# Kernel tuning notes

Hardware: AMD Instinct MI355X
Metric: run time of the kernel (lower is better)

Reference implementation:

```python
import jax, jax.numpy as jnp
import numpy as np

B, T, E, H = 4, 4096, 1024, 64

def setup_inputs() -> dict:
    key = jax.random.key(0)
    k1, k2, k3, k4 = jax.random.split(key, 4)
    x = jax.random.normal(k1, (B, T, E), dtype=jnp.float32)
    # nn.Linear(E, H, bias=False): weight [H, E]; store as [E, H] for x @ W
    scale = 1.0 / np.sqrt(E)
    Wk = jax.random.normal(k2, (E, H), dtype=jnp.float32) * scale
    Wq = jax.random.normal(k3, (E, H), dtype=jnp.float32) * scale
    Wv = jax.random.normal(k4, (E, H), dtype=jnp.float32) * scale
    return {"x": x, "Wk": Wk, "Wq": Wq, "Wv": Wv}

def reference(x, Wk, Wq, Wv):
    Bc, Tc, Ec = x.shape
    k = x @ Wk            # [B, T, H]
    q = x @ Wq            # [B, T, H]
    v = x @ Wv            # [B, T, H]
    # NOTE: original scales by 1/sqrt(embedding_size), not head_size
    scores = jnp.einsum('bqh,bkh->bqk', q, k) / jnp.sqrt(jnp.float32(Ec))
    causal = jnp.tril(jnp.ones((Tc, Tc), dtype=bool))
    scores = jnp.where(causal, scores, -jnp.inf)
    weights = jax.nn.softmax(scores, axis=-1)
    return jnp.einsum('bqk,bkh->bqh', weights, v)
```

## Files before the change

### kernel.cpp

```cpp
#include <hip/hip_runtime.h>

#define B_ 4
#define T_ 4096
#define E_ 1024
#define H_ 64

typedef __attribute__((ext_vector_type(8))) short short8;
typedef __attribute__((ext_vector_type(4))) float f32x4;

static __device__ __forceinline__ unsigned short f2bf(float f) {
    unsigned int u = __builtin_bit_cast(unsigned int, f);
    u += 0x7fffu + ((u >> 16) & 1u);
    return (unsigned short)(u >> 16);
}
static __device__ __forceinline__ float bf2f(unsigned short h) {
    unsigned int u = ((unsigned int)h) << 16;
    return __builtin_bit_cast(float, u);
}
#if __has_builtin(__builtin_amdgcn_exp2f)
#define EXP2(x) __builtin_amdgcn_exp2f(x)
#else
#define EXP2(x) exp2f(x)
#endif

#define GLOBAL_AS __attribute__((address_space(1)))
#define LDS_AS    __attribute__((address_space(3)))

__global__ __launch_bounds__(256) void wt_transpose_kernel(
    const float* __restrict__ Wq, const float* __restrict__ Wk,
    const float* __restrict__ Wv, unsigned short* __restrict__ Wt)
{
    __shared__ float tile[64][65];
    const int mat = blockIdx.x >> 4;
    const int kt  = blockIdx.x & 15;
    const float* W = (mat == 0) ? Wq : ((mat == 1) ? Wk : Wv);
    const int tid = threadIdx.x;
    #pragma unroll
    for (int p = 0; p < 16; ++p) {
        int idx = p * 256 + tid;
        tile[idx >> 6][idx & 63] = W[(kt * 64 + (idx >> 6)) * 64 + (idx & 63)];
    }
    __syncthreads();
    #pragma unroll
    for (int p = 0; p < 16; ++p) {
        int idx = p * 256 + tid;
        int h = idx >> 6, kl = idx & 63;
        Wt[(mat * 64 + h) * E_ + kt * 64 + kl] = f2bf(tile[kl][h]);
    }
}

__global__ __launch_bounds__(768, 1) void proj_kernel(
    const float* __restrict__ x, const unsigned short* __restrict__ Wt,
    unsigned short* __restrict__ Qb, unsigned short* __restrict__ Kb,
    unsigned short* __restrict__ Vt)
{
    __shared__ float          x_lds[2][4096];
    __shared__ unsigned short wt_lds[2][12288];
    const int tid  = threadIdx.x;
    const int wid  = tid >> 6, lane = tid & 63;
    const int g    = lane >> 4, c = lane & 15;
    const int mat  = wid >> 2;
    const int rg   = wid & 3;
    const int r0   = blockIdx.x * 64;
    const float QSCALE = 0.03125f * 1.44269504088896f;

    auto stage = [&](int buf, int kk) {
        {
            int row = tid >> 4, ch = tid & 15;
            int csw = ch ^ (row & 15);
            const float* src = x + (size_t)(r0 + row) * E_ + kk + csw * 4;
            __builtin_amdgcn_global_load_lds(
                (const GLOBAL_AS unsigned int*)src,
                (LDS_AS unsigned int*)&x_lds[buf][(tid & ~63) * 4], 16, 0, 0);
            if (tid < 256) {
                int idx2 = 768 + tid;
                int row2 = idx2 >> 4, ch2 = idx2 & 15;
                int csw2 = ch2 ^ (row2 & 15);
                const float* src2 = x + (size_t)(r0 + row2) * E_ + kk + csw2 * 4;
                __builtin_amdgcn_global_load_lds(
                    (const GLOBAL_AS unsigned int*)src2,
                    (LDS_AS unsigned int*)&x_lds[buf][(idx2 & ~63) * 4], 16, 0, 0);
            }
        }
        #pragma unroll
        for (int p = 0; p < 2; ++p) {
            int idx = p * 768 + tid;
            int row = idx >> 3, ch = idx & 7;
            int csw = ch ^ (row & 7);
            const unsigned short* src = Wt + (size_t)row * E_ + kk + csw * 8;
            __builtin_amdgcn_global_load_lds(
                (const GLOBAL_AS unsigned int*)src,
                (LDS_AS unsigned int*)&wt_lds[buf][(idx & ~63) * 8], 16, 0, 0);
        }
    };

    f32x4 acc[4];
    #pragma unroll
    for (int n = 0; n < 4; ++n) acc[n] = 0.0f;

    stage(0, 0);
    __syncthreads();

    for (int t = 0; t < 16; ++t) {
        const int buf = t & 1;
        if (t < 15) stage(buf ^ 1, (t + 1) * 64);

        const int xrowbase = (rg * 16 + c) * 64;
        const int wrowbase = (mat * 64 + c) * 64;
        #pragma unroll
        for (int kc = 0; kc < 2; ++kc) {
            f32x4 xa = *(const f32x4*)&x_lds[buf][xrowbase + ((8 * kc + 2 * g)     ^ c) * 4];
            f32x4 xb = *(const f32x4*)&x_lds[buf][xrowbase + ((8 * kc + 2 * g + 1) ^ c) * 4];
            short8 a;
            #pragma unroll
            for (int j = 0; j < 4; ++j) {
                a[j]     = (short)f2bf(xa[j]);
                a[j + 4] = (short)f2bf(xb[j]);
            }
            #pragma unroll
            for (int n = 0; n < 4; ++n) {
                short8 b = *(const short8*)
                    &wt_lds[buf][wrowbase + n * 1024 + (((4 * kc + g) ^ (c & 7)) * 8)];
                acc[n] = __builtin_amdgcn_mfma_f32_16x16x32_bf16(a, b, acc[n], 0, 0, 0);
            }
        }
        __syncthreads();
    }

    const int bb = r0 >> 12;
    #pragma unroll
    for (int n = 0; n < 4; ++n)
        #pragma unroll
        for (int r = 0; r < 4; ++r) {
            int row = r0 + rg * 16 + 4 * g + r;
            int col = n * 16 + c;
            float v = acc[n][r];
            if (mat == 0)
                Qb[(size_t)row * H_ + col] = f2bf(v * QSCALE);
            else if (mat == 1)
                Kb[(size_t)row * H_ + col] = f2bf(v);
            else
                Vt[((size_t)bb * H_ + col) * T_ + (row & (T_ - 1))] = f2bf(v);
        }
}

__global__ __launch_bounds__(256, 3) void attn_split_kernel(
    const unsigned short* __restrict__ Qb, const unsigned short* __restrict__ Kb,
    const unsigned short* __restrict__ Vt, unsigned short* __restrict__ Po,
    float* __restrict__ Pl)
{
    __shared__ unsigned short K_lds[2][64][64];
    __shared__ unsigned short V_lds[2][64][64];
    __shared__ unsigned short p_lds[4][16][72];
    const int tid   = threadIdx.x;
    const int wid   = tid >> 6, lane = tid & 63;
    const int g     = lane >> 4, c = lane & 15;

    const int s     = blockIdx.x * 4 + wid;
    const int batch = s >> 11;
    const int rem   = s & 2047;
    const int ch    = rem >> 8;
    const int qt    = rem & 255;
    const int nkv   = (qt >> 2) + 1;
    if (ch * 8 >= nkv) return;
    const int nt    = min(8, nkv - ch * 8);
    const int qbase = qt * 16;
    const int lastt = nkv - 1 - ch * 8;

    const int Mm = nkv - 1, aa = Mm >> 3, rr8 = Mm & 7;
    const int npart = (nkv + 7) >> 3;
    const int slot  = batch * 1152 + 4 * (4 * aa * (aa + 1) + rr8 * (aa + 1))
                    + (qt & 3) * npart + ch;

    const int rsub = lane >> 3;
    const int csw  = (lane & 7) ^ rsub;
    const int cs0 = (g ^ (c & 7)) * 8;
    const int cs1 = ((g + 4) ^ (c & 7)) * 8;

    short8 aq0, aq1;
    {
        const unsigned short* qp = Qb + ((size_t)(batch * T_ + qbase + c)) * H_ + 8 * g;
        aq0 = *(const short8*)&qp[0];
        aq1 = *(const short8*)&qp[32];
    }

    short8 ones;
    #pragma unroll
    for (int j = 0; j < 8; ++j) ones[j] = (short)0x3F80;

    f32x4 o_acc[4];
    #pragma unroll
    for (int n = 0; n < 4; ++n) o_acc[n] = 0.0f;
    f32x4 l_acc = 0.0f;

    auto stage = [&](int buf, int gt) {
        const int key0 = gt * 64;
        #pragma unroll
        for (int j = 0; j < 2; ++j) {
            const int row = wid * 16 + j * 8;
            const unsigned short* gk = Kb
                + ((size_t)(batch * T_ + key0 + row + rsub)) * H_ + csw * 8;
            __builtin_amdgcn_global_load_lds(
                (const GLOBAL_AS unsigned int*)gk,
                (LDS_AS unsigned int*)&K_lds[buf][row][0], 16, 0, 0);
            const unsigned short* gv = Vt
                + ((size_t)(batch * H_ + row + rsub)) * T_ + key0 + csw * 8;
            __builtin_amdgcn_global_load_lds(
                (const GLOBAL_AS unsigned int*)gv,
                (LDS_AS unsigned int*)&V_lds[buf][row][0], 16, 0, 0);
        }
    };

    stage(0, ch * 8);
    __syncthreads();

    for (int t = 0; t < nt; ++t) {
        const int buf = t & 1;
        if (t + 1 < nt) stage(buf ^ 1, ch * 8 + t + 1);

        f32x4 sA[4];
        #pragma unroll
        for (int n = 0; n < 4; ++n) sA[n] = 0.0f;
        #pragma unroll
        for (int n = 0; n < 4; ++n) {
            short8 bk0 = *(const short8*)&K_lds[buf][n * 16 + c][cs0];
            short8 bk1 = *(const short8*)&K_lds[buf][n * 16 + c][cs1];
            sA[n] = __builtin_amdgcn_mfma_f32_16x16x32_bf16(aq0, bk0, sA[n], 0, 0, 0);
            sA[n] = __builtin_amdgcn_mfma_f32_16x16x32_bf16(aq1, bk1, sA[n], 0, 0, 0);
        }

        float pv[4][4];
        #pragma unroll
        for (int n = 0; n < 4; ++n)
            #pragma unroll
            for (int r = 0; r < 4; ++r)
                pv[n][r] = EXP2(sA[n][r]);
        if (t == lastt) {
            const int d = (ch * 8 + t) * 64 + c - qbase - 4 * g;
            #pragma unroll
            for (int n = 0; n < 4; ++n)
                #pragma unroll
                for (int r = 0; r < 4; ++r)
                    if (d + 16 * n > r) pv[n][r] = 0.0f;
        }

        #pragma unroll
        for (int n = 0; n < 4; ++n)
            #pragma unroll
            for (int r = 0; r < 4; ++r)
                p_lds[wid][4 * g + r][n * 16 + c] = f2bf(pv[n][r]);
        short8 pa0 = *(const short8*)&p_lds[wid][c][8 * g];
        short8 pa1 = *(const short8*)&p_lds[wid][c][32 + 8 * g];

        l_acc = __builtin_amdgcn_mfma_f32_16x16x32_bf16(pa0, ones, l_acc, 0, 0, 0);
        l_acc = __builtin_amdgcn_mfma_f32_16x16x32_bf16(pa1, ones, l_acc, 0, 0, 0);

        #pragma unroll
        for (int n = 0; n < 4; ++n) {
            short8 bv0 = *(const short8*)&V_lds[buf][n * 16 + c][cs0];
            short8 bv1 = *(const short8*)&V_lds[buf][n * 16 + c][cs1];
            o_acc[n] = __builtin_amdgcn_mfma_f32_16x16x32_bf16(pa0, bv0, o_acc[n], 0, 0, 0);
            o_acc[n] = __builtin_amdgcn_mfma_f32_16x16x32_bf16(pa1, bv1, o_acc[n], 0, 0, 0);
        }

        __syncthreads();
    }

    unsigned short* po = Po + (size_t)slot * 1024;
    #pragma unroll
    for (int n = 0; n < 4; ++n)
        #pragma unroll
        for (int r = 0; r < 4; ++r)
            po[(4 * g + r) * 64 + n * 16 + c] = f2bf(o_acc[n][r]);
    if (c == 0) {
        #pragma unroll
        for (int r = 0; r < 4; ++r)
            Pl[slot * 16 + 4 * g + r] = l_acc[r];
    }
}

__global__ __launch_bounds__(256) void attn_merge_kernel(
    const unsigned short* __restrict__ Po, const float* __restrict__ Pl,
    float* __restrict__ out)
{
    const int tid  = threadIdx.x;
    const int wid  = tid >> 6, lane = tid & 63;
    const int gi   = blockIdx.x * 4 + wid;
    const int batch = gi >> 8, qt = gi & 255;
    const int nkv  = (qt >> 2) + 1;
    const int npart = (nkv + 7) >> 3;
    const int Mm = nkv - 1, aa = Mm >> 3, rr8 = Mm & 7;
    const int slot0 = batch * 1152 + 4 * (4 * aa * (aa + 1) + rr8 * (aa + 1))
                    + (qt & 3) * npart;

    const int row = lane & 15, seg = lane >> 4;

    float lacc = 0.0f, o[16];
    #pragma unroll
    for (int k = 0; k < 16; ++k) o[k] = 0.0f;

    for (int i = 0; i < npart; ++i) {
        lacc += Pl[(slot0 + i) * 16 + row];
        const unsigned short* pp = Po + (size_t)(slot0 + i) * 1024 + row * 64 + seg * 16;
        short8 v0 = *(const short8*)&pp[0];
        short8 v1 = *(const short8*)&pp[8];
        #pragma unroll
        for (int k = 0; k < 8; ++k) {
            o[k]     += bf2f((unsigned short)v0[k]);
            o[8 + k] += bf2f((unsigned short)v1[k]);
        }
    }

    const float inv = 1.0f / lacc;
    float* op = out + ((size_t)(batch * T_ + qt * 16 + row)) * H_ + seg * 16;
    #pragma unroll
    for (int k = 0; k < 16; ++k) op[k] = o[k] * inv;
}

extern "C" void kernel_launch(void* const* d_in, const int* in_sizes, int n_in,
                              void* d_out, int out_size, void* d_ws, size_t ws_size,
                              hipStream_t stream)
{
    const float* x  = (const float*)d_in[0];
    const float* Wk = (const float*)d_in[1];
    const float* Wq = (const float*)d_in[2];
    const float* Wv = (const float*)d_in[3];
    float* out = (float*)d_out;

    unsigned short* Wt = (unsigned short*)d_ws;
    unsigned short* Qb = Wt + 3 * 64 * 1024;
    unsigned short* Kb = Qb + (size_t)B_ * T_ * H_;
    unsigned short* Vt = Kb + (size_t)B_ * T_ * H_;
    unsigned short* Po = Vt + (size_t)B_ * T_ * H_;
    float* Pl = (float*)(Po + (size_t)4608 * 1024);

    hipLaunchKernelGGL(wt_transpose_kernel, dim3(48), dim3(256), 0, stream, Wq, Wk, Wv, Wt);
    hipLaunchKernelGGL(proj_kernel, dim3(256), dim3(768), 0, stream, x, Wt, Qb, Kb, Vt);
    hipLaunchKernelGGL(attn_split_kernel, dim3(2048), dim3(256), 0, stream, Qb, Kb, Vt, Po, Pl);
    hipLaunchKernelGGL(attn_merge_kernel, dim3(256), dim3(256), 0, stream, Po, Pl, out);
}
```

Measured before the change: 67.94 us.

## Load x directly into registers and pipeline weight staging with manual waitcnt

The projection kernel stops staging x through LDS and has each wave load its x rows from global memory straight into registers, double-buffered one step ahead. Weight tiles are still staged in LDS, and the loop is unrolled by two with explicit s_waitcnt vmcnt and s_barrier in place of __syncthreads. This cuts LDS traffic and barrier cost, but each x row is now fetched by the three matrix waves separately, which adds global/L2 reads.

```diff
diff --git a/kernel.cpp b/kernel.cpp
--- a/kernel.cpp
+++ b/kernel.cpp
@@ -54,7 +54,6 @@
     unsigned short* __restrict__ Qb, unsigned short* __restrict__ Kb,
     unsigned short* __restrict__ Vt)
 {
-    __shared__ float          x_lds[2][4096];
     __shared__ unsigned short wt_lds[2][12288];
     const int tid  = threadIdx.x;
     const int wid  = tid >> 6, lane = tid & 63;
@@ -64,24 +63,9 @@
     const int r0   = blockIdx.x * 64;
     const float QSCALE = 0.03125f * 1.44269504088896f;
 
-    auto stage = [&](int buf, int kk) {
-        {
-            int row = tid >> 4, ch = tid & 15;
-            int csw = ch ^ (row & 15);
-            const float* src = x + (size_t)(r0 + row) * E_ + kk + csw * 4;
-            __builtin_amdgcn_global_load_lds(
-                (const GLOBAL_AS unsigned int*)src,
-                (LDS_AS unsigned int*)&x_lds[buf][(tid & ~63) * 4], 16, 0, 0);
-            if (tid < 256) {
-                int idx2 = 768 + tid;
-                int row2 = idx2 >> 4, ch2 = idx2 & 15;
-                int csw2 = ch2 ^ (row2 & 15);
-                const float* src2 = x + (size_t)(r0 + row2) * E_ + kk + csw2 * 4;
-                __builtin_amdgcn_global_load_lds(
-                    (const GLOBAL_AS unsigned int*)src2,
-                    (LDS_AS unsigned int*)&x_lds[buf][(idx2 & ~63) * 4], 16, 0, 0);
-            }
-        }
+    const float* xrow = x + (size_t)(r0 + rg * 16 + c) * E_;
+
+    auto stageWt = [&](int buf, int kk) {
         #pragma unroll
         for (int p = 0; p < 2; ++p) {
             int idx = p * 768 + tid;
@@ -93,29 +77,27 @@
                 (LDS_AS unsigned int*)&wt_lds[buf][(idx & ~63) * 8], 16, 0, 0);
         }
     };
+    auto loadx = [&](f32x4* dst, int t) {
+        const float* xr = xrow + t * 64;
+        dst[0] = *(const f32x4*)&xr[8 * g];
+        dst[1] = *(const f32x4*)&xr[8 * g + 4];
+        dst[2] = *(const f32x4*)&xr[32 + 8 * g];
+        dst[3] = *(const f32x4*)&xr[32 + 8 * g + 4];
+    };
 
     f32x4 acc[4];
     #pragma unroll
     for (int n = 0; n < 4; ++n) acc[n] = 0.0f;
 
-    stage(0, 0);
-    __syncthreads();
-
-    for (int t = 0; t < 16; ++t) {
-        const int buf = t & 1;
-        if (t < 15) stage(buf ^ 1, (t + 1) * 64);
-
-        const int xrowbase = (rg * 16 + c) * 64;
-        const int wrowbase = (mat * 64 + c) * 64;
+    const int wrowbase = (mat * 64 + c) * 64;
+    auto computeStep = [&](int buf, const f32x4* xs) {
         #pragma unroll
         for (int kc = 0; kc < 2; ++kc) {
-            f32x4 xa = *(const f32x4*)&x_lds[buf][xrowbase + ((8 * kc + 2 * g)     ^ c) * 4];
-            f32x4 xb = *(const f32x4*)&x_lds[buf][xrowbase + ((8 * kc + 2 * g + 1) ^ c) * 4];
             short8 a;
             #pragma unroll
             for (int j = 0; j < 4; ++j) {
-                a[j]     = (short)f2bf(xa[j]);
-                a[j + 4] = (short)f2bf(xb[j]);
+                a[j]     = (short)f2bf(xs[kc * 2][j]);
+                a[j + 4] = (short)f2bf(xs[kc * 2 + 1][j]);
             }
             #pragma unroll
             for (int n = 0; n < 4; ++n) {
@@ -124,7 +106,31 @@
                 acc[n] = __builtin_amdgcn_mfma_f32_16x16x32_bf16(a, b, acc[n], 0, 0, 0);
             }
         }
-        __syncthreads();
+    };
+
+    f32x4 xA[4], xB[4];
+    stageWt(0, 0);
+    asm volatile("" ::: "memory");
+    loadx(xA, 0);
+    asm volatile("s_waitcnt vmcnt(0)\n\ts_barrier" ::: "memory");
+
+    #pragma unroll
+    for (int tt = 0; tt < 16; tt += 2) {
+        stageWt(1, (tt + 1) * 64);
+        asm volatile("" ::: "memory");
+        loadx(xB, tt + 1);
+        computeStep(0, xA);
+        asm volatile("s_waitcnt vmcnt(4)\n\ts_barrier" ::: "memory");
+
+        if (tt + 2 < 16) {
+            stageWt(0, (tt + 2) * 64);
+            asm volatile("" ::: "memory");
+            loadx(xA, tt + 2);
+            computeStep(1, xB);
+            asm volatile("s_waitcnt vmcnt(4)\n\ts_barrier" ::: "memory");
+        } else {
+            computeStep(1, xB);
+        }
     }
 
     const int bb = r0 >> 12;
```

New measurement: 74.11 us. 9.1% more time.

## Split projection GEMM along K into two halves with a merge kernel

Applied to the files above, without the earlier changes.

The projection kernel now splits the 1024-wide reduction into two halves, doubling the grid from 256 to 512 blocks so more CUs get work. Each half writes bf16 partial sums to workspace, and a new merge kernel adds them, applies the Q scale and writes Q, K and transposed V. This costs an extra kernel launch, an extra round trip of partials through memory, and an extra bf16 rounding of the partial sums. The launch-bounds hint also changes.

```diff
diff --git a/kernel.cpp b/kernel.cpp
--- a/kernel.cpp
+++ b/kernel.cpp
@@ -49,10 +49,9 @@
     }
 }
 
-__global__ __launch_bounds__(768, 1) void proj_kernel(
+__global__ __launch_bounds__(768, 6) void proj_kernel(
     const float* __restrict__ x, const unsigned short* __restrict__ Wt,
-    unsigned short* __restrict__ Qb, unsigned short* __restrict__ Kb,
-    unsigned short* __restrict__ Vt)
+    unsigned short* __restrict__ Pp)
 {
     __shared__ float          x_lds[2][4096];
     __shared__ unsigned short wt_lds[2][12288];
@@ -61,8 +60,10 @@
     const int g    = lane >> 4, c = lane & 15;
     const int mat  = wid >> 2;
     const int rg   = wid & 3;
-    const int r0   = blockIdx.x * 64;
-    const float QSCALE = 0.03125f * 1.44269504088896f;
+    const int mtile = blockIdx.x >> 1;
+    const int kh    = blockIdx.x & 1;
+    const int r0   = mtile * 64;
+    const int k0   = kh * 512;
 
     auto stage = [&](int buf, int kk) {
         {
@@ -98,15 +99,9 @@
     #pragma unroll
     for (int n = 0; n < 4; ++n) acc[n] = 0.0f;
 
-    stage(0, 0);
-    __syncthreads();
-
-    for (int t = 0; t < 16; ++t) {
-        const int buf = t & 1;
-        if (t < 15) stage(buf ^ 1, (t + 1) * 64);
-
-        const int xrowbase = (rg * 16 + c) * 64;
-        const int wrowbase = (mat * 64 + c) * 64;
+    const int xrowbase = (rg * 16 + c) * 64;
+    const int wrowbase = (mat * 64 + c) * 64;
+    auto computeStep = [&](int buf) {
         #pragma unroll
         for (int kc = 0; kc < 2; ++kc) {
             f32x4 xa = *(const f32x4*)&x_lds[buf][xrowbase + ((8 * kc + 2 * g)     ^ c) * 4];
@@ -124,24 +119,60 @@
                 acc[n] = __builtin_amdgcn_mfma_f32_16x16x32_bf16(a, b, acc[n], 0, 0, 0);
             }
         }
+    };
+
+    stage(0, k0);
+    __syncthreads();
+    for (int t = 0; t < 8; ++t) {
+        const int buf = t & 1;
+        if (t + 1 < 8) stage(buf ^ 1, k0 + (t + 1) * 64);
+        computeStep(buf);
         __syncthreads();
     }
 
-    const int bb = r0 >> 12;
+    unsigned short* pp = Pp + ((size_t)kh * 16384 + r0) * 192;
     #pragma unroll
     for (int n = 0; n < 4; ++n)
         #pragma unroll
-        for (int r = 0; r < 4; ++r) {
-            int row = r0 + rg * 16 + 4 * g + r;
-            int col = n * 16 + c;
-            float v = acc[n][r];
-            if (mat == 0)
-                Qb[(size_t)row * H_ + col] = f2bf(v * QSCALE);
-            else if (mat == 1)
-                Kb[(size_t)row * H_ + col] = f2bf(v);
-            else
-                Vt[((size_t)bb * H_ + col) * T_ + (row & (T_ - 1))] = f2bf(v);
-        }
+        for (int r = 0; r < 4; ++r)
+            pp[(rg * 16 + 4 * g + r) * 192 + mat * 64 + n * 16 + c] = f2bf(acc[n][r]);
+}
+
+__global__ __launch_bounds__(256) void qkv_merge_kernel(
+    const unsigned short* __restrict__ Pp,
+    unsigned short* __restrict__ Qb, unsigned short* __restrict__ Kb,
+    unsigned short* __restrict__ Vt)
+{
+    const float QSCALE = 0.03125f * 1.44269504088896f;
+    const int idx   = blockIdx.x * 256 + threadIdx.x;
+    const int row   = idx / 24;
+    const int chunk = idx - row * 24;
+
+    short8 a = *(const short8*)&Pp[(size_t)row * 192 + chunk * 8];
+    short8 b = *(const short8*)&Pp[((size_t)16384 + row) * 192 + chunk * 8];
+    float s[8];
+    #pragma unroll
+    for (int j = 0; j < 8; ++j)
+        s[j] = bf2f((unsigned short)a[j]) + bf2f((unsigned short)b[j]);
+
+    if (chunk < 8) {
+        short8 v;
+        #pragma unroll
+        for (int j = 0; j < 8; ++j) v[j] = (short)f2bf(s[j] * QSCALE);
+        *(short8*)&Qb[(size_t)row * H_ + chunk * 8] = v;
+    } else if (chunk < 16) {
+        short8 v;
+        #pragma unroll
+        for (int j = 0; j < 8; ++j) v[j] = (short)f2bf(s[j]);
+        *(short8*)&Kb[(size_t)row * H_ + (chunk - 8) * 8] = v;
+    } else {
+        const int col0 = (chunk - 16) * 8;
+        const int bb   = row >> 12;
+        const int rloc = row & (T_ - 1);
+        #pragma unroll
+        for (int j = 0; j < 8; ++j)
+            Vt[((size_t)(bb * H_ + col0 + j)) * T_ + rloc] = f2bf(s[j]);
+    }
 }
 
 __global__ __launch_bounds__(256, 3) void attn_split_kernel(
@@ -331,11 +362,14 @@
     unsigned short* Qb = Wt + 3 * 64 * 1024;
     unsigned short* Kb = Qb + (size_t)B_ * T_ * H_;
     unsigned short* Vt = Kb + (size_t)B_ * T_ * H_;
-    unsigned short* Po = Vt + (size_t)B_ * T_ * H_;
+    unsigned short* U  = Vt + (size_t)B_ * T_ * H_;
+    unsigned short* Pp = U;
+    unsigned short* Po = U;
     float* Pl = (float*)(Po + (size_t)4608 * 1024);
 
     hipLaunchKernelGGL(wt_transpose_kernel, dim3(48), dim3(256), 0, stream, Wq, Wk, Wv, Wt);
-    hipLaunchKernelGGL(proj_kernel, dim3(256), dim3(768), 0, stream, x, Wt, Qb, Kb, Vt);
+    hipLaunchKernelGGL(proj_kernel, dim3(512), dim3(768), 0, stream, x, Wt, Pp);
+    hipLaunchKernelGGL(qkv_merge_kernel, dim3(1536), dim3(256), 0, stream, Pp, Qb, Kb, Vt);
     hipLaunchKernelGGL(attn_split_kernel, dim3(2048), dim3(256), 0, stream, Qb, Kb, Vt, Po, Pl);
     hipLaunchKernelGGL(attn_merge_kernel, dim3(256), dim3(256), 0, stream, Po, Pl, out);
 }
```

Result: faster. 64.72 us (-4.7%).

## Split projection kernel into per-matrix 256-thread blocks for more parallelism

Applied to the files above, without the earlier changes.

The fused 768-thread block that computed Q, K and V for a 64-row tile becomes three 256-thread blocks, one per weight matrix. The grid grows from 256 to 768 blocks, which fills more CUs on the chip and allows up to three blocks per CU, with smaller LDS per block. The cost is that each x tile is loaded from global memory three times instead of once, tripling x traffic for the projection.

```diff
diff --git a/kernel.cpp b/kernel.cpp
--- a/kernel.cpp
+++ b/kernel.cpp
@@ -49,45 +49,38 @@
     }
 }
 
-__global__ __launch_bounds__(768, 1) void proj_kernel(
+__global__ __launch_bounds__(256, 3) void proj_kernel(
     const float* __restrict__ x, const unsigned short* __restrict__ Wt,
     unsigned short* __restrict__ Qb, unsigned short* __restrict__ Kb,
     unsigned short* __restrict__ Vt)
 {
     __shared__ float          x_lds[2][4096];
-    __shared__ unsigned short wt_lds[2][12288];
+    __shared__ unsigned short wt_lds[2][4096];
     const int tid  = threadIdx.x;
-    const int wid  = tid >> 6, lane = tid & 63;
+    const int rg   = tid >> 6, lane = tid & 63;
     const int g    = lane >> 4, c = lane & 15;
-    const int mat  = wid >> 2;
-    const int rg   = wid & 3;
-    const int r0   = blockIdx.x * 64;
+    const int bx   = blockIdx.x;
+    const int mtile = bx / 3, mat = bx - mtile * 3;
+    const int r0   = mtile * 64;
     const float QSCALE = 0.03125f * 1.44269504088896f;
 
     auto stage = [&](int buf, int kk) {
-        {
-            int row = tid >> 4, ch = tid & 15;
+        #pragma unroll
+        for (int p = 0; p < 4; ++p) {
+            int idx = p * 256 + tid;
+            int row = idx >> 4, ch = idx & 15;
             int csw = ch ^ (row & 15);
             const float* src = x + (size_t)(r0 + row) * E_ + kk + csw * 4;
             __builtin_amdgcn_global_load_lds(
                 (const GLOBAL_AS unsigned int*)src,
-                (LDS_AS unsigned int*)&x_lds[buf][(tid & ~63) * 4], 16, 0, 0);
-            if (tid < 256) {
-                int idx2 = 768 + tid;
-                int row2 = idx2 >> 4, ch2 = idx2 & 15;
-                int csw2 = ch2 ^ (row2 & 15);
-                const float* src2 = x + (size_t)(r0 + row2) * E_ + kk + csw2 * 4;
-                __builtin_amdgcn_global_load_lds(
-                    (const GLOBAL_AS unsigned int*)src2,
-                    (LDS_AS unsigned int*)&x_lds[buf][(idx2 & ~63) * 4], 16, 0, 0);
-            }
+                (LDS_AS unsigned int*)&x_lds[buf][(idx & ~63) * 4], 16, 0, 0);
         }
         #pragma unroll
         for (int p = 0; p < 2; ++p) {
-            int idx = p * 768 + tid;
+            int idx = p * 256 + tid;
             int row = idx >> 3, ch = idx & 7;
             int csw = ch ^ (row & 7);
-            const unsigned short* src = Wt + (size_t)row * E_ + kk + csw * 8;
+            const unsigned short* src = Wt + (size_t)(mat * 64 + row) * E_ + kk + csw * 8;
             __builtin_amdgcn_global_load_lds(
                 (const GLOBAL_AS unsigned int*)src,
                 (LDS_AS unsigned int*)&wt_lds[buf][(idx & ~63) * 8], 16, 0, 0);
@@ -98,15 +91,8 @@
     #pragma unroll
     for (int n = 0; n < 4; ++n) acc[n] = 0.0f;
 
-    stage(0, 0);
-    __syncthreads();
-
-    for (int t = 0; t < 16; ++t) {
-        const int buf = t & 1;
-        if (t < 15) stage(buf ^ 1, (t + 1) * 64);
-
-        const int xrowbase = (rg * 16 + c) * 64;
-        const int wrowbase = (mat * 64 + c) * 64;
+    const int xrowbase = (rg * 16 + c) * 64;
+    auto computeStep = [&](int buf) {
         #pragma unroll
         for (int kc = 0; kc < 2; ++kc) {
             f32x4 xa = *(const f32x4*)&x_lds[buf][xrowbase + ((8 * kc + 2 * g)     ^ c) * 4];
@@ -120,10 +106,18 @@
             #pragma unroll
             for (int n = 0; n < 4; ++n) {
                 short8 b = *(const short8*)
-                    &wt_lds[buf][wrowbase + n * 1024 + (((4 * kc + g) ^ (c & 7)) * 8)];
+                    &wt_lds[buf][(n * 16 + c) * 64 + (((4 * kc + g) ^ (c & 7)) * 8)];
                 acc[n] = __builtin_amdgcn_mfma_f32_16x16x32_bf16(a, b, acc[n], 0, 0, 0);
             }
         }
+    };
+
+    stage(0, 0);
+    __syncthreads();
+    for (int t = 0; t < 16; ++t) {
+        const int buf = t & 1;
+        if (t + 1 < 16) stage(buf ^ 1, (t + 1) * 64);
+        computeStep(buf);
         __syncthreads();
     }
 
@@ -335,7 +329,7 @@
     float* Pl = (float*)(Po + (size_t)4608 * 1024);
 
     hipLaunchKernelGGL(wt_transpose_kernel, dim3(48), dim3(256), 0, stream, Wq, Wk, Wv, Wt);
-    hipLaunchKernelGGL(proj_kernel, dim3(256), dim3(768), 0, stream, x, Wt, Qb, Kb, Vt);
+    hipLaunchKernelGGL(proj_kernel, dim3(768), dim3(256), 0, stream, x, Wt, Qb, Kb, Vt);
     hipLaunchKernelGGL(attn_split_kernel, dim3(2048), dim3(256), 0, stream, Qb, Kb, Vt, Po, Pl);
     hipLaunchKernelGGL(attn_merge_kernel, dim3(256), dim3(256), 0, stream, Po, Pl, out);
 }
```

Result: slower. 76.98 us (+13.3%).
